# Performance work log

Measured on AMD Instinct MI355X. Metric: run time of the kernel, lower is better.

The kernel has to match this reference:

```python
import jax, jax.numpy as jnp
import numpy as np

B, T, F, H = 64, 512, 132, 1024


def setup_inputs() -> dict:
    key = jax.random.key(0)
    ks = jax.random.split(key, 16)
    k = 1.0 / np.sqrt(H)
    u = lambda kk, shape: jax.random.uniform(kk, shape, jnp.float32, -k, k)
    return {
        "real_seq": jax.random.normal(ks[0], (B, T, F), jnp.float32),
        "Wih1": u(ks[1], (4 * H, F)), "Whh1": u(ks[2], (4 * H, H)),
        "bih1": u(ks[3], (4 * H,)), "bhh1": u(ks[4], (4 * H,)),
        "Wih2": u(ks[5], (4 * H, H)), "Whh2": u(ks[6], (4 * H, H)),
        "bih2": u(ks[7], (4 * H,)), "bhh2": u(ks[8], (4 * H,)),
        "Wih3": u(ks[9], (4 * H, H)), "Whh3": u(ks[10], (4 * H, H)),
        "bih3": u(ks[11], (4 * H,)), "bhh3": u(ks[12], (4 * H,)),
        "Wd": u(ks[13], (F, H)), "bd": u(ks[14], (F,)),
        "condition_num": 5, "groundtruth_num": 5,
    }


def _cell(x, h, c, Wih, Whh, bih, bhh):
    # torch LSTMCell gate order: i, f, g, o
    gates = x @ Wih.T + h @ Whh.T + bih + bhh
    i, f, g, o = jnp.split(gates, 4, axis=-1)
    c_new = jax.nn.sigmoid(f) * c + jax.nn.sigmoid(i) * jnp.tanh(g)
    h_new = jax.nn.sigmoid(o) * jnp.tanh(c_new)
    return h_new, c_new


def reference(real_seq, Wih1, Whh1, bih1, bhh1, Wih2, Whh2, bih2, bhh2,
              Wih3, Whh3, bih3, bhh3, Wd, bd, condition_num, groundtruth_num):
    batch, seq_len, _ = real_seq.shape
    hid = Whh1.shape[1]
    out_dim = Wd.shape[0]
    # static teacher-forcing schedule (numpy, as in get_condition_lst)
    gt = np.ones((100, groundtruth_num))
    con = np.zeros((100, condition_num))
    cond = jnp.asarray(np.concatenate((gt, con), 1).reshape(-1)[:seq_len],
                       jnp.float32)

    def step(carry, xs):
        h0, h1, h2, c0, c1, c2, prev_out = carry
        frame, flag = xs
        in_frame = jnp.where(flag == 1.0, frame, prev_out)
        # NOTE: faithful to source -- lstm2 gets OLD h0, lstm3 gets OLD h1
        h0n, c0n = _cell(in_frame, h0, c0, Wih1, Whh1, bih1, bhh1)
        h1n, c1n = _cell(h0, h1, c1, Wih2, Whh2, bih2, bhh2)
        h2n, c2n = _cell(h1, h2, c2, Wih3, Whh3, bih3, bhh3)
        out = h2n @ Wd.T + bd
        return (h0n, h1n, h2n, c0n, c1n, c2n, out), out

    z = jnp.zeros((batch, hid), real_seq.dtype)
    out0 = jnp.zeros((batch, out_dim), real_seq.dtype)
    _, outs = jax.lax.scan(step, (z, z, z, z, z, z, out0),
                           (jnp.swapaxes(real_seq, 0, 1), cond))
    # outs: [T, B, F] -> concat along feature axis per timestep: [B, T*F]
    return jnp.transpose(outs, (1, 0, 2)).reshape(batch, seq_len * out_dim)
```

## Files before the change

kernel.cpp:

```cpp
#include <hip/hip_runtime.h>
#include <cstdint>


#define NBLK 256
#define NTHR 512
#define Bn 64
#define Tn 512
#define Fn 132
#define Hn 1024
#define TF (Tn * Fn)
#define SRCH 65536
#define HBUF 196608
#define XTT 10240
#define WPB 102400
#define STB 393216
#define STU 49152

typedef _Float16 h8 __attribute__((ext_vector_type(8)));
typedef float f4 __attribute__((ext_vector_type(4)));
typedef int v4i __attribute__((ext_vector_type(4)));
typedef unsigned long long ull;

__device__ v4i llvm_amdgcn_raw_buffer_load_v4i32(v4i srsrc, int voffset,
                                                 int soffset, int aux)
    __asm("llvm.amdgcn.raw.buffer.load.v4i32");

__device__ __forceinline__ v4i make_srd(const void* p) {
    union { struct { unsigned lo, hi, sz, cfg; } s; v4i v; } u;
    u.s.lo = (unsigned)(uintptr_t)p;
    u.s.hi = (unsigned)((uintptr_t)p >> 32);
    u.s.sz = 0xFFFFFFFFu;
    u.s.cfg = 0x00020000u;
    return u.v;
}

__device__ __forceinline__ h8 bload16(v4i rsrc, int voff) {
    union { v4i i; h8 h; } c;
    c.i = llvm_amdgcn_raw_buffer_load_v4i32(rsrc, voff, 0, 1 );
    return c.h;
}

__device__ __forceinline__ float sigf(float x) { return 1.0f / (1.0f + expf(-x)); }

__device__ __forceinline__ ull cload8(const void* p) {
    return __hip_atomic_load((const ull*)p, __ATOMIC_RELAXED, __HIP_MEMORY_SCOPE_AGENT);
}
__device__ __forceinline__ void cstore8(void* p, ull v) {
    __hip_atomic_store((ull*)p, v, __ATOMIC_RELAXED, __HIP_MEMORY_SCOPE_AGENT);
}

__device__ __forceinline__ void garrive(unsigned* bar, unsigned ep) {
    unsigned* cnt = bar + ((blockIdx.x >> 5) << 5);
    unsigned old = __hip_atomic_fetch_add(cnt, 1u, __ATOMIC_RELAXED,
                                          __HIP_MEMORY_SCOPE_AGENT);
    if (old == 32u * ep - 1u) {
        unsigned d = __hip_atomic_fetch_add(bar + 256, 1u, __ATOMIC_RELAXED,
                                            __HIP_MEMORY_SCOPE_AGENT);
        if (d == 8u * ep - 1u)
            __hip_atomic_store(bar + 288, ep, __ATOMIC_RELAXED,
                               __HIP_MEMORY_SCOPE_AGENT);
    }
}
__device__ __forceinline__ void gwait(unsigned* bar, unsigned ep) {
    while (__hip_atomic_load(bar + 288, __ATOMIC_RELAXED,
                             __HIP_MEMORY_SCOPE_AGENT) < ep)
        __builtin_amdgcn_s_sleep(1);
}
__device__ __forceinline__ void gsyncA(unsigned* bar, unsigned ep) {
    __syncthreads();
    if (threadIdx.x == 0) { garrive(bar, ep); gwait(bar, ep); }
    __syncthreads();
}


__global__ void k_bsum(const float* bih1, const float* bhh1, const float* bih2,
                       const float* bhh2, const float* bih3, const float* bhh3,
                       const float* Wih1, const float* bd,
                       float* bsum, float* bsum2) {
    int i = blockIdx.x * 256 + threadIdx.x;
    if (i < NBLK * 48) {
        int bidw = i / 48, r = i % 48;
        int cell = r >> 4, n = r & 15;
        int row = (n >> 2) * Hn + bidw * 4 + (n & 3);
        const float* bi = cell == 0 ? bih1 : (cell == 1 ? bih2 : bih3);
        const float* bh = cell == 0 ? bhh1 : (cell == 1 ? bhh2 : bhh3);
        bsum[i] = bi[row] + bh[row];
    } else if (i < NBLK * 64) {
        int ii = i - NBLK * 48;
        int bidw = ii / 16, n = ii % 16;
        int row = (n >> 2) * Hn + bidw * 4 + (n & 3);
        float s = 0.0f;
        for (int f = 0; f < Fn; ++f) s += Wih1[(size_t)row * Fn + f] * bd[f];
        bsum2[bidw * 16 + n] = s;
    }
}

__global__ void k_convx(const float* xseq, _Float16* xT) {
    int i = blockIdx.x * 256 + threadIdx.x;
    if (i >= Tn * XTT) return;
    int t = i / XTT, r = i % XTT;
    int k8 = r >> 9, b = (r >> 3) & 63, e = r & 7;
    int f = k8 * 8 + e;
    float v = (f < Fn) ? xseq[((size_t)b * Tn + t) * Fn + f] : 0.0f;
    xT[i] = (_Float16)v;
}

__global__ void k_convw(const float* Wih1, const float* Whh1, const float* Wih2,
                        const float* Whh2, const float* Wih3, const float* Whh3,
                        const float* Wd, _Float16* wblob) {
    int i = blockIdx.x * 256 + threadIdx.x;
    if (i >= NBLK * WPB) return;
    int bidw = i / WPB, r = i % WPB;
    int slot = r >> 9, e = r & 511;
    int w = slot / 25, s = slot - w * 25;
    int l = e >> 3, j = e & 7;
    int kq = l >> 4, n = l & 15;
    int row = (n >> 2) * Hn + bidw * 4 + (n & 3);
    float v = 0.0f;
    if (s >= 21) {
        int kt = w * 4 + (s - 21);
        int k = kt * 32 + kq * 8 + j;
        float acc = 0.0f;
        for (int f = 0; f < Fn; ++f)
            acc += Wih1[(size_t)row * Fn + f] * Wd[(size_t)f * Hn + k];
        v = acc;
    } else {
        const float* M;
        int K, kt;
        if (s < 4)       { M = Whh1; K = Hn; kt = w * 4 + s; }
        else if (s < 8)  { M = Wih2; K = Hn; kt = w * 4 + s - 4; }
        else if (s < 12) { M = Whh2; K = Hn; kt = w * 4 + s - 8; }
        else if (s < 16) { M = Wih3; K = Hn; kt = w * 4 + s - 12; }
        else if (s < 20) { M = Whh3; K = Hn; kt = w * 4 + s - 16; }
        else             { M = Wih1; K = Fn; kt = w; }
        int k = kt * 32 + kq * 8 + j;
        if (!(s == 20 && w >= 5) && k < K) v = M[(size_t)row * K + k];
    }
    wblob[i] = (_Float16)v;
}

__global__ void k_misc(_Float16* hT) {
    int i = blockIdx.x * 256 + threadIdx.x;
    if (i < HBUF) hT[i] = (_Float16)0.0f;
}


__global__ __launch_bounds__(NTHR, 2) void lstm_mfma(
    const _Float16* __restrict__ xT, const _Float16* __restrict__ wblob,
    _Float16* __restrict__ hT, unsigned char* __restrict__ xstage,
    const float* __restrict__ bsum, const float* __restrict__ bsum2,
    const float* __restrict__ Wd, const float* __restrict__ bd,
    const int* __restrict__ cnum_p, const int* __restrict__ gnum_p,
    float* __restrict__ dout, unsigned* __restrict__ bar) {
    __shared__ float red[8 * 12 * 68 * 4];
    __shared__ float cst[768];
    __shared__ float sbias[48];
    __shared__ float sbias2[16];
    __shared__ unsigned long long hstage[192];
    __shared__ int sxi[3];

    const int tid = threadIdx.x;
    const int bid = blockIdx.x;
    const int lane = tid & 63;
    const int wid = tid >> 6;
    const int laneAB = (lane >> 4) * 1024 + (lane & 15) * 16;
    const int laneA0 = (lane >> 4) * 512 + (lane & 15) * 8;
    const int widB = wid * 16384;

    if (tid < 48) sbias[tid] = bsum[bid * 48 + tid];
    if (tid >= 64 && tid < 80) sbias2[tid - 64] = bsum2[bid * 16 + (tid - 64)];
    for (int i = tid; i < 768; i += NTHR) cst[i] = 0.0f;

    h8 wfr[25];
    {
        const _Float16* wp = wblob + (size_t)bid * WPB + (size_t)(wid * 25) * 512 + lane * 8;
#pragma unroll
        for (int s2 = 0; s2 < 25; ++s2) wfr[s2] = *(const h8*)(wp + s2 * 512);
    }

    if (tid == 0) {
        unsigned x;
        asm volatile("s_getreg_b32 %0, hwreg(HW_REG_XCC_ID)" : "=s"(x));
        x &= 7u;
        unsigned r = __hip_atomic_fetch_add(bar + 384 + x * 16, 1u,
                                            __ATOMIC_RELAXED, __HIP_MEMORY_SCOPE_AGENT);
        sxi[0] = (int)x; sxi[1] = (int)r;
    }
    gsyncA(bar, 1);
    if (tid == 0)
        sxi[2] = (int)__hip_atomic_load(bar + 384 + sxi[0] * 16, __ATOMIC_RELAXED,
                                        __HIP_MEMORY_SCOPE_AGENT);
    __syncthreads();
    const int xcd = sxi[0], xrank = sxi[1], xN = sxi[2];
    unsigned* xb = bar + 640 + xcd * 16;
    unsigned char* xsb = xstage + (size_t)xcd * 2 * STB;

    const int gnum = gnum_p[0];
    const int per = gnum + cnum_p[0];

    auto decoder = [&](v4i rsrc, int tt) {
        const int ss = tid >> 6, b = tid & 63;
        const int nj = (bid < 8) ? 2 : 1;
        for (int j2 = 0; j2 < nj; ++j2) {
            int f, half;
            if (j2 == 0) {
                if (bid < Fn) { f = bid; half = 0; }
                else          { f = bid - Fn; half = 1; }
            } else { f = bid + (NBLK - Fn); half = 1; }
            const float* wdr = Wd + (size_t)f * Hn;
            h8 hv[8];
#pragma unroll
            for (int i = 0; i < 8; ++i) {
                const int k8 = half * 64 + ss * 8 + i;
                hv[i] = bload16(rsrc, 262144 + k8 * 1024 + b * 16);
            }
            float p = 0.0f;
#pragma unroll
            for (int i = 0; i < 8; ++i) {
                const int k8 = half * 64 + ss * 8 + i;
                const float4 w0 = *(const float4*)(wdr + k8 * 8);
                const float4 w1 = *(const float4*)(wdr + k8 * 8 + 4);
                p = fmaf((float)hv[i][0], w0.x, p); p = fmaf((float)hv[i][1], w0.y, p);
                p = fmaf((float)hv[i][2], w0.z, p); p = fmaf((float)hv[i][3], w0.w, p);
                p = fmaf((float)hv[i][4], w1.x, p); p = fmaf((float)hv[i][5], w1.y, p);
                p = fmaf((float)hv[i][6], w1.z, p); p = fmaf((float)hv[i][7], w1.w, p);
            }
            red[ss * 64 + b] = p;
            __syncthreads();
            if (tid < 64) {
                float o = (half == 0) ? bd[f] : 0.0f;
#pragma unroll
                for (int u = 0; u < 8; ++u) o += red[u * 64 + tid];
                unsafeAtomicAdd(&dout[(size_t)tid * TF + (size_t)tt * Fn + f], o);
            }
            __syncthreads();
        }
    };

    auto stageT = [&](int rbuf, int slot) {
        const ull* src = (const ull*)(hT + (size_t)rbuf * HBUF);
        ull* dst = (ull*)(xsb + (size_t)slot * STB);
        for (int s2 = xrank; s2 < 32; s2 += xN) {
            const int u = s2 * 1536 + tid;
#pragma unroll
            for (int q = 0; q < 3; ++q)
                dst[u + q * 512] = cload8(src + u + q * 512);
        }
        __syncthreads();
    };
    auto xarrive = [&]() {
        if (tid == 0)
            __hip_atomic_fetch_add(xb, 1u, __ATOMIC_RELAXED, __HIP_MEMORY_SCOPE_AGENT);
    };
    auto xpoll = [&](unsigned target) {
        if (tid == 0)
            while (__hip_atomic_load(xb, __ATOMIC_RELAXED, __HIP_MEMORY_SCOPE_AGENT) < target)
                __builtin_amdgcn_s_sleep(1);
        __syncthreads();
    };

    int tmod = 0;
    for (int t = 0; t < Tn; ++t) {
        const int flag = (tmod < gnum) ? 1 : 0;
        const bool fused = (!flag) && (t > 0);
        const int rb = t % 3, wb2 = (t + 1) % 3;
        _Float16* hw = hT + (size_t)wb2 * HBUF;

        const ull* ssrc = (const ull*)(hT + (size_t)rb * HBUF);
        ull* sdst = (ull*)(xsb + (size_t)(t & 1) * STB);
        ull sv0 = 0, sv1 = 0, sv2 = 0;
        int u0 = -1;
        if (xrank < 32) {
            u0 = xrank * 1536 + tid;
            sv0 = cload8(ssrc + u0);
            sv1 = cload8(ssrc + u0 + 512);
            sv2 = cload8(ssrc + u0 + 1024);
        }
        f4 acc[12];
#pragma unroll
        for (int i = 0; i < 12; ++i) acc[i] = (f4){0.f, 0.f, 0.f, 0.f};
        if (u0 >= 0) { sdst[u0] = sv0; sdst[u0 + 512] = sv1; sdst[u0 + 1024] = sv2; }
        for (int s2 = xrank + xN; s2 < 32; s2 += xN) {
            const int u = s2 * 1536 + tid;
#pragma unroll
            for (int q = 0; q < 3; ++q)
                sdst[u + q * 512] = cload8(ssrc + u + q * 512);
        }
        __syncthreads();
        xarrive();

        if (flag && wid < 5) {
            const _Float16* x0 = xT + (size_t)t * XTT + wid * 2048 + laneA0;
            h8 xa[4];
#pragma unroll
            for (int mt = 0; mt < 4; ++mt) xa[mt] = *(const h8*)(x0 + mt * 128);
#pragma unroll
            for (int mt = 0; mt < 4; ++mt)
                acc[mt] = __builtin_amdgcn_mfma_f32_16x16x32_f16(xa[mt], wfr[20], acc[mt], 0, 0, 0);
        }
        xpoll((unsigned)(xN * (t + 1)));
        const v4i rsrc = make_srd(xsb + (size_t)(t & 1) * STB);

        {
            h8 a[16];
#pragma unroll
            for (int i2 = 0; i2 < 4; ++i2)
#pragma unroll
                for (int mt = 0; mt < 4; ++mt)
                    a[i2 * 4 + mt] = bload16(rsrc, widB + i2 * 4096 + mt * 256 + laneAB);
#pragma unroll
            for (int i2 = 0; i2 < 4; ++i2)
#pragma unroll
                for (int mt = 0; mt < 4; ++mt) {
                    acc[mt]     = __builtin_amdgcn_mfma_f32_16x16x32_f16(a[i2 * 4 + mt], wfr[i2],     acc[mt],     0, 0, 0);
                    acc[4 + mt] = __builtin_amdgcn_mfma_f32_16x16x32_f16(a[i2 * 4 + mt], wfr[4 + i2], acc[4 + mt], 0, 0, 0);
                }
        }
        {
            h8 a[16];
#pragma unroll
            for (int i2 = 0; i2 < 4; ++i2)
#pragma unroll
                for (int mt = 0; mt < 4; ++mt)
                    a[i2 * 4 + mt] = bload16(rsrc, 131072 + widB + i2 * 4096 + mt * 256 + laneAB);
#pragma unroll
            for (int i2 = 0; i2 < 4; ++i2)
#pragma unroll
                for (int mt = 0; mt < 4; ++mt) {
                    acc[4 + mt] = __builtin_amdgcn_mfma_f32_16x16x32_f16(a[i2 * 4 + mt], wfr[8 + i2],  acc[4 + mt], 0, 0, 0);
                    acc[8 + mt] = __builtin_amdgcn_mfma_f32_16x16x32_f16(a[i2 * 4 + mt], wfr[12 + i2], acc[8 + mt], 0, 0, 0);
                }
        }
        {
            h8 a[16];
#pragma unroll
            for (int i2 = 0; i2 < 4; ++i2)
#pragma unroll
                for (int mt = 0; mt < 4; ++mt)
                    a[i2 * 4 + mt] = bload16(rsrc, 262144 + widB + i2 * 4096 + mt * 256 + laneAB);
            if (fused) {
#pragma unroll
                for (int i2 = 0; i2 < 4; ++i2)
#pragma unroll
                    for (int mt = 0; mt < 4; ++mt) {
                        acc[8 + mt] = __builtin_amdgcn_mfma_f32_16x16x32_f16(a[i2 * 4 + mt], wfr[16 + i2], acc[8 + mt], 0, 0, 0);
                        acc[mt]     = __builtin_amdgcn_mfma_f32_16x16x32_f16(a[i2 * 4 + mt], wfr[21 + i2], acc[mt],     0, 0, 0);
                    }
            } else {
#pragma unroll
                for (int i2 = 0; i2 < 4; ++i2)
#pragma unroll
                    for (int mt = 0; mt < 4; ++mt)
                        acc[8 + mt] = __builtin_amdgcn_mfma_f32_16x16x32_f16(a[i2 * 4 + mt], wfr[16 + i2], acc[8 + mt], 0, 0, 0);
            }
        }

        {
            float* wr = red + ((size_t)(wid * 12) * 68 + (lane >> 4) * 17 + (lane & 15)) * 4;
#pragma unroll
            for (int cc = 0; cc < 3; ++cc)
#pragma unroll
                for (int mt = 0; mt < 4; ++mt)
                    *(f4*)(wr + (cc * 4 + mt) * 68 * 4) = acc[cc * 4 + mt];
        }
        __syncthreads();
        const float bmul = fused ? 1.0f : 0.0f;
        for (int idx = tid; idx < 768; idx += NTHR) {
            const int cell = idx >> 8, jj = (idx >> 6) & 3, b = idx & 63;
            const int mt = b >> 4, mq = (b >> 2) & 3, rr = b & 3;
            float gv4[4];
#pragma unroll
            for (int gt = 0; gt < 4; ++gt) {
                const int n = gt * 4 + jj;
                float v = sbias[cell * 16 + n];
                if (cell == 0) v += bmul * sbias2[n];
#pragma unroll
                for (int w2 = 0; w2 < 8; ++w2)
                    v += red[(((w2 * 12 + cell * 4 + mt)) * 68 + mq * 17 + n) * 4 + rr];
                gv4[gt] = v;
            }
            const float cold = cst[(cell * 4 + jj) * 64 + b];
            const float cn = sigf(gv4[1]) * cold + sigf(gv4[0]) * tanhf(gv4[2]);
            cst[(cell * 4 + jj) * 64 + b] = cn;
            const float hn = sigf(gv4[3]) * tanhf(cn);
            ((_Float16*)hstage)[(cell * 64 + b) * 4 + jj] = (_Float16)hn;
        }
        __syncthreads();
        if (tid < 192) {
            const int cell = tid >> 6, b = tid & 63;
            _Float16* dst = hw + cell * SRCH + (bid >> 1) * 512 + b * 8 + 4 * (bid & 1);
            cstore8(dst, hstage[tid]);
        }

        __syncthreads();
        if (tid == 0) garrive(bar, (unsigned)(t + 2));
        if (t > 0) decoder(rsrc, t - 1);
        __syncthreads();
        if (tid == 0) gwait(bar, (unsigned)(t + 2));
        __syncthreads();

        tmod = (tmod + 1 >= per) ? 0 : (tmod + 1);
    }

    stageT(Tn % 3, Tn & 1);
    if (tid == 0) {
        __hip_atomic_fetch_add(xb, 1u, __ATOMIC_RELAXED, __HIP_MEMORY_SCOPE_AGENT);
        while (__hip_atomic_load(xb, __ATOMIC_RELAXED, __HIP_MEMORY_SCOPE_AGENT)
               < (unsigned)(xN * (Tn + 1)))
            __builtin_amdgcn_s_sleep(1);
    }
    __syncthreads();
    decoder(make_srd(xsb + (size_t)(Tn & 1) * STB), Tn - 1);
}


extern "C" void kernel_launch(void* const* d_in, const int* in_sizes, int n_in,
                              void* d_out, int out_size, void* d_ws, size_t ws_size,
                              hipStream_t stream) {
    const float* xseq = (const float*)d_in[0];
    const float* Wih1 = (const float*)d_in[1];
    const float* Whh1 = (const float*)d_in[2];
    const float* bih1 = (const float*)d_in[3];
    const float* bhh1 = (const float*)d_in[4];
    const float* Wih2 = (const float*)d_in[5];
    const float* Whh2 = (const float*)d_in[6];
    const float* bih2 = (const float*)d_in[7];
    const float* bhh2 = (const float*)d_in[8];
    const float* Wih3 = (const float*)d_in[9];
    const float* Whh3 = (const float*)d_in[10];
    const float* bih3 = (const float*)d_in[11];
    const float* bhh3 = (const float*)d_in[12];
    const float* Wd = (const float*)d_in[13];
    const float* bd = (const float*)d_in[14];
    const int* cnum_p = (const int*)d_in[15];
    const int* gnum_p = (const int*)d_in[16];

    unsigned char* ws = (unsigned char*)d_ws;
    unsigned* bar = (unsigned*)ws;
    float* bsum = (float*)(ws + 4096);
    float* bsum2 = (float*)(ws + 53248);
    _Float16* xT = (_Float16*)(ws + 102400);
    _Float16* wblob = (_Float16*)(ws + 102400 + 10485760);
    _Float16* hT = (_Float16*)(ws + 102400 + 10485760 + 52428800);
    unsigned char* xstage = ws + 102400 + 10485760 + 52428800 + 1179648;

    hipMemsetAsync(bar, 0, 4096, stream);
    hipMemsetAsync(d_out, 0, (size_t)out_size * sizeof(float), stream);
    hipLaunchKernelGGL(k_bsum, dim3((NBLK * 64 + 255) / 256), dim3(256), 0, stream,
                       bih1, bhh1, bih2, bhh2, bih3, bhh3, Wih1, bd, bsum, bsum2);
    hipLaunchKernelGGL(k_convx, dim3((Tn * XTT + 255) / 256), dim3(256), 0, stream,
                       xseq, xT);
    hipLaunchKernelGGL(k_convw, dim3((NBLK * WPB + 255) / 256), dim3(256), 0, stream,
                       Wih1, Whh1, Wih2, Whh2, Wih3, Whh3, Wd, wblob);
    hipLaunchKernelGGL(k_misc, dim3((HBUF + 255) / 256), dim3(256), 0, stream, hT);
    hipLaunchKernelGGL(lstm_mfma, dim3(NBLK), dim3(NTHR), 0, stream,
                       xT, wblob, hT, xstage, bsum, bsum2, Wd, bd, cnum_p, gnum_p,
                       (float*)d_out, bar);
}
```

Baseline: 7.791 ms.

## Drop per-XCD staging copy of hidden state; read global buffer directly

Removes the per-XCD staging scheme in which the blocks on each XCD cooperatively copied the hidden-state ring buffer into an XCD-local staging area and synchronized on an XCD counter before reading it. Blocks now issue an agent-scope acquire fence and buffer-load directly from the global hT ring slot. The initial XCD-discovery barrier is removed, so the global barrier epochs shift by one. This cuts a copy and an extra intra-XCD sync per timestep, but every block now pulls the full hidden state from global memory, which may miss the local L2 more often across XCDs.

```diff
diff --git a/kernel.cpp b/kernel.cpp
--- a/kernel.cpp
+++ b/kernel.cpp
@@ -13,8 +13,6 @@
 #define HBUF 196608
 #define XTT 10240
 #define WPB 102400
-#define STB 393216
-#define STU 49152
 
 typedef _Float16 h8 __attribute__((ext_vector_type(8)));
 typedef float f4 __attribute__((ext_vector_type(4)));
@@ -42,9 +40,6 @@
 
 __device__ __forceinline__ float sigf(float x) { return 1.0f / (1.0f + expf(-x)); }
 
-__device__ __forceinline__ ull cload8(const void* p) {
-    return __hip_atomic_load((const ull*)p, __ATOMIC_RELAXED, __HIP_MEMORY_SCOPE_AGENT);
-}
 __device__ __forceinline__ void cstore8(void* p, ull v) {
     __hip_atomic_store((ull*)p, v, __ATOMIC_RELAXED, __HIP_MEMORY_SCOPE_AGENT);
 }
@@ -65,11 +60,6 @@
     while (__hip_atomic_load(bar + 288, __ATOMIC_RELAXED,
                              __HIP_MEMORY_SCOPE_AGENT) < ep)
         __builtin_amdgcn_s_sleep(1);
-}
-__device__ __forceinline__ void gsyncA(unsigned* bar, unsigned ep) {
-    __syncthreads();
-    if (threadIdx.x == 0) { garrive(bar, ep); gwait(bar, ep); }
-    __syncthreads();
 }
 
 
@@ -157,7 +147,6 @@
     __shared__ float sbias[48];
     __shared__ float sbias2[16];
     __shared__ unsigned long long hstage[192];
-    __shared__ int sxi[3];
 
     const int tid = threadIdx.x;
     const int bid = blockIdx.x;
@@ -177,23 +166,7 @@
 #pragma unroll
         for (int s2 = 0; s2 < 25; ++s2) wfr[s2] = *(const h8*)(wp + s2 * 512);
     }
-
-    if (tid == 0) {
-        unsigned x;
-        asm volatile("s_getreg_b32 %0, hwreg(HW_REG_XCC_ID)" : "=s"(x));
-        x &= 7u;
-        unsigned r = __hip_atomic_fetch_add(bar + 384 + x * 16, 1u,
-                                            __ATOMIC_RELAXED, __HIP_MEMORY_SCOPE_AGENT);
-        sxi[0] = (int)x; sxi[1] = (int)r;
-    }
-    gsyncA(bar, 1);
-    if (tid == 0)
-        sxi[2] = (int)__hip_atomic_load(bar + 384 + sxi[0] * 16, __ATOMIC_RELAXED,
-                                        __HIP_MEMORY_SCOPE_AGENT);
     __syncthreads();
-    const int xcd = sxi[0], xrank = sxi[1], xN = sxi[2];
-    unsigned* xb = bar + 640 + xcd * 16;
-    unsigned char* xsb = xstage + (size_t)xcd * 2 * STB;
 
     const int gnum = gnum_p[0];
     const int per = gnum + cnum_p[0];
@@ -237,28 +210,6 @@
         }
     };
 
-    auto stageT = [&](int rbuf, int slot) {
-        const ull* src = (const ull*)(hT + (size_t)rbuf * HBUF);
-        ull* dst = (ull*)(xsb + (size_t)slot * STB);
-        for (int s2 = xrank; s2 < 32; s2 += xN) {
-            const int u = s2 * 1536 + tid;
-#pragma unroll
-            for (int q = 0; q < 3; ++q)
-                dst[u + q * 512] = cload8(src + u + q * 512);
-        }
-        __syncthreads();
-    };
-    auto xarrive = [&]() {
-        if (tid == 0)
-            __hip_atomic_fetch_add(xb, 1u, __ATOMIC_RELAXED, __HIP_MEMORY_SCOPE_AGENT);
-    };
-    auto xpoll = [&](unsigned target) {
-        if (tid == 0)
-            while (__hip_atomic_load(xb, __ATOMIC_RELAXED, __HIP_MEMORY_SCOPE_AGENT) < target)
-                __builtin_amdgcn_s_sleep(1);
-        __syncthreads();
-    };
-
     int tmod = 0;
     for (int t = 0; t < Tn; ++t) {
         const int flag = (tmod < gnum) ? 1 : 0;
@@ -266,28 +217,12 @@
         const int rb = t % 3, wb2 = (t + 1) % 3;
         _Float16* hw = hT + (size_t)wb2 * HBUF;
 
-        const ull* ssrc = (const ull*)(hT + (size_t)rb * HBUF);
-        ull* sdst = (ull*)(xsb + (size_t)(t & 1) * STB);
-        ull sv0 = 0, sv1 = 0, sv2 = 0;
-        int u0 = -1;
-        if (xrank < 32) {
-            u0 = xrank * 1536 + tid;
-            sv0 = cload8(ssrc + u0);
-            sv1 = cload8(ssrc + u0 + 512);
-            sv2 = cload8(ssrc + u0 + 1024);
-        }
+        __builtin_amdgcn_fence(__ATOMIC_ACQUIRE, "agent");
+        const v4i rsrc = make_srd(hT + (size_t)rb * HBUF);
+
         f4 acc[12];
 #pragma unroll
         for (int i = 0; i < 12; ++i) acc[i] = (f4){0.f, 0.f, 0.f, 0.f};
-        if (u0 >= 0) { sdst[u0] = sv0; sdst[u0 + 512] = sv1; sdst[u0 + 1024] = sv2; }
-        for (int s2 = xrank + xN; s2 < 32; s2 += xN) {
-            const int u = s2 * 1536 + tid;
-#pragma unroll
-            for (int q = 0; q < 3; ++q)
-                sdst[u + q * 512] = cload8(ssrc + u + q * 512);
-        }
-        __syncthreads();
-        xarrive();
 
         if (flag && wid < 5) {
             const _Float16* x0 = xT + (size_t)t * XTT + wid * 2048 + laneA0;
@@ -298,8 +233,6 @@
             for (int mt = 0; mt < 4; ++mt)
                 acc[mt] = __builtin_amdgcn_mfma_f32_16x16x32_f16(xa[mt], wfr[20], acc[mt], 0, 0, 0);
         }
-        xpoll((unsigned)(xN * (t + 1)));
-        const v4i rsrc = make_srd(xsb + (size_t)(t & 1) * STB);
 
         {
             h8 a[16];
@@ -393,24 +326,17 @@
         }
 
         __syncthreads();
-        if (tid == 0) garrive(bar, (unsigned)(t + 2));
+        if (tid == 0) garrive(bar, (unsigned)(t + 1));
         if (t > 0) decoder(rsrc, t - 1);
         __syncthreads();
-        if (tid == 0) gwait(bar, (unsigned)(t + 2));
+        if (tid == 0) gwait(bar, (unsigned)(t + 1));
         __syncthreads();
 
         tmod = (tmod + 1 >= per) ? 0 : (tmod + 1);
     }
 
-    stageT(Tn % 3, Tn & 1);
-    if (tid == 0) {
-        __hip_atomic_fetch_add(xb, 1u, __ATOMIC_RELAXED, __HIP_MEMORY_SCOPE_AGENT);
-        while (__hip_atomic_load(xb, __ATOMIC_RELAXED, __HIP_MEMORY_SCOPE_AGENT)
-               < (unsigned)(xN * (Tn + 1)))
-            __builtin_amdgcn_s_sleep(1);
-    }
-    __syncthreads();
-    decoder(make_srd(xsb + (size_t)(Tn & 1) * STB), Tn - 1);
+    __builtin_amdgcn_fence(__ATOMIC_ACQUIRE, "agent");
+    decoder(make_srd(hT + (size_t)(Tn % 3) * HBUF), Tn - 1);
 }
 
 
```

Result: slower. 12.92 ms (+65.9%).
